# Kernel optimization log

Hardware: AMD Instinct MI355X
Metric: run time of the kernel (lower is better)

## Reference

```python
import jax, jax.numpy as jnp
import numpy as np

EPSILON = 1e-8
DT = 0.1
STEPS = 3
MASK_DENSITY = 0.01


def setup_inputs() -> dict:
    key = jax.random.key(0)
    k1, k2 = jax.random.split(key)
    B, S, D = 4, 4096, 2
    psi = jax.random.normal(k1, (B, S, D), dtype=jnp.float32)
    # binary mask: threshold a uniform draw to get a sparse 0/1 adjacency
    u = jax.random.uniform(k2, (B, S, S), dtype=jnp.float32)
    binary_mask = (u < MASK_DENSITY).astype(jnp.float32)
    return {"psi": psi, "binary_mask": binary_mask}


def reference(psi, binary_mask):
    def force(state):
        # adjacency-weighted aggregation minus self: [B,S,S] @ [B,S,2]
        return jnp.einsum('bij,bjd->bid', binary_mask, state) - state

    def step(p, _):
        r = jnp.linalg.norm(p, axis=-1, keepdims=True)          # [B,S,1]
        k1 = force(p)
        psi_star = p + DT * k1
        star_norm = jnp.linalg.norm(psi_star, axis=-1, keepdims=True)
        psi_star = psi_star * (r / (star_norm + EPSILON))       # renormalize to r
        k2 = force(psi_star)
        p_new = p + 0.5 * DT * (k1 + k2)
        new_norm = jnp.linalg.norm(p_new, axis=-1, keepdims=True)
        p_new = p_new * (r / (new_norm + EPSILON))              # norm-preserving
        return p_new, None

    psi_out, _ = jax.lax.scan(step, psi, None, length=STEPS)
    return psi_out
```

## Files before the change

kernel.cpp:

```cpp
#include <hip/hip_runtime.h>
#include <stdint.h>

#define BATCH   4
#define SEQ     4096
#define WPR     64
#define NROWS   (BATCH * SEQ)
#define CAP     256
#define DTS     0.1f
#define HALF_DT 0.05f
#define EPS     1e-8f

__device__ __forceinline__ float2 ballot_force_sum(unsigned long long w,
                                                   const float2* __restrict__ gb,
                                                   int lane) {
    const int colbase = ((lane >> 2) << 8) | (lane & 3);
    float sx = 0.f, sy = 0.f;
    while (w) {
        int j = __builtin_ctzll(w);
        w &= (w - 1);
        float2 v = gb[colbase + (j << 2)];
        sx += v.x; sy += v.y;
    }
#pragma unroll
    for (int m = 32; m >= 1; m >>= 1) {
        sx += __shfl_xor(sx, m, 64);
        sy += __shfl_xor(sy, m, 64);
    }
    return make_float2(sx, sy);
}

__global__ __launch_bounds__(256)
void compress_phaseA(const float* __restrict__ mask,
                     const float2* __restrict__ psi,
                     ushort* __restrict__ idx,
                     int*    __restrict__ cnt,
                     float2* __restrict__ k1buf,
                     float2* __restrict__ starbuf,
                     float*  __restrict__ rbuf) {
    const int row  = (blockIdx.x * blockDim.x + threadIdx.x) >> 6;
    const int lane = threadIdx.x & 63;

    const float4* src = reinterpret_cast<const float4*>(mask + (size_t)row * SEQ);
    unsigned long long word = 0ull;
#pragma unroll
    for (int c = 0; c < 16; ++c) {
        float4 v = src[c * 64 + lane];
        unsigned long long b;
        b = __ballot(v.x != 0.f); if (lane == c * 4 + 0) word = b;
        b = __ballot(v.y != 0.f); if (lane == c * 4 + 1) word = b;
        b = __ballot(v.z != 0.f); if (lane == c * 4 + 2) word = b;
        b = __ballot(v.w != 0.f); if (lane == c * 4 + 3) word = b;
    }

    int pc  = __popcll(word);
    int inc = pc;
#pragma unroll
    for (int ofs = 1; ofs < 64; ofs <<= 1) {
        int t = __shfl_up(inc, ofs, 64);
        if (lane >= ofs) inc += t;
    }
    int pos   = inc - pc;
    int total = __shfl(inc, 63, 64);

    ushort* dst = idx + ((size_t)row << 8);
    const int colbase = ((lane >> 2) << 8) | (lane & 3);
    unsigned long long w = word;
    while (w) {
        int j = __builtin_ctzll(w);
        w &= (w - 1);
        if (pos < CAP) dst[pos] = (ushort)(colbase + (j << 2));
        ++pos;
    }
    if (lane == 0) cnt[row] = total > CAP ? CAP : total;

    const int bidx = row >> 12;
    float2 sum = ballot_force_sum(word, psi + ((size_t)bidx << 12), lane);
    float2 p  = psi[row];
    float r   = sqrtf(p.x * p.x + p.y * p.y);
    float k1x = sum.x - p.x, k1y = sum.y - p.y;
    float tx  = p.x + DTS * k1x, ty = p.y + DTS * k1y;
    float sc  = r / (sqrtf(tx * tx + ty * ty) + EPS);
    if (lane == 0) {
        k1buf[row]   = make_float2(k1x, k1y);
        starbuf[row] = make_float2(tx * sc, ty * sc);
        rbuf[row]    = r;
    }
}

template <int PHASE>
__global__ __launch_bounds__(256)
void force_step(const ushort* __restrict__ idx,
                const int*    __restrict__ cnt,
                const float2* __restrict__ pIn,
                const float2* __restrict__ gsrc,
                float2* __restrict__ k1buf,
                float2* __restrict__ starbuf,
                float*  __restrict__ rbuf,
                float2* __restrict__ outbuf) {
    const int tid = blockIdx.x * blockDim.x + threadIdx.x;
    const int row = tid >> 4;
    const int q   = tid & 15;
    const int bidx = row >> 12;
    const float2* __restrict__ gb = gsrc + ((size_t)bidx << 12);

    const int n = cnt[row];
    const ushort* __restrict__ ip = idx + ((size_t)row << 8);

    float sx = 0.f, sy = 0.f;
    int i = q;
    for (; i + 16 < n; i += 32) {
        int c0 = ip[i];
        int c1 = ip[i + 16];
        float2 v0 = gb[c0];
        float2 v1 = gb[c1];
        sx += v0.x + v1.x;
        sy += v0.y + v1.y;
    }
    if (i < n) {
        int c = ip[i];
        float2 v = gb[c];
        sx += v.x; sy += v.y;
    }
#pragma unroll
    for (int m = 8; m >= 1; m >>= 1) {
        sx += __shfl_xor(sx, m, 64);
        sy += __shfl_xor(sy, m, 64);
    }

    if (q == 0) {
        if (PHASE == 0) {
            float2 p = pIn[row];
            float r   = sqrtf(p.x * p.x + p.y * p.y);
            float k1x = sx - p.x, k1y = sy - p.y;
            float tx  = p.x + DTS * k1x, ty = p.y + DTS * k1y;
            float sc  = r / (sqrtf(tx * tx + ty * ty) + EPS);
            k1buf[row]   = make_float2(k1x, k1y);
            starbuf[row] = make_float2(tx * sc, ty * sc);
            rbuf[row]    = r;
        } else {
            float2 st = gsrc[row];
            float k2x = sx - st.x, k2y = sy - st.y;
            float2 p  = pIn[row];
            float2 k1 = k1buf[row];
            float nx  = p.x + HALF_DT * (k1.x + k2x);
            float ny  = p.y + HALF_DT * (k1.y + k2y);
            float sc  = rbuf[row] / (sqrtf(nx * nx + ny * ny) + EPS);
            outbuf[row] = make_float2(nx * sc, ny * sc);
        }
    }
}

extern "C" void kernel_launch(void* const* d_in, const int* in_sizes, int n_in,
                              void* d_out, int out_size, void* d_ws, size_t ws_size,
                              hipStream_t stream) {
    const float* psi  = (const float*)d_in[0];
    const float* mask = (const float*)d_in[1];
    float2* out2 = (float2*)d_out;

    char* ws = (char*)d_ws;
    ushort* idx = (ushort*)ws;
    int*    cnt = (int*)(ws + (size_t)NROWS * CAP * sizeof(ushort));
    float2* p    = (float2*)((char*)cnt + (size_t)NROWS * sizeof(int));
    float2* k1   = p + NROWS;
    float2* star = k1 + NROWS;
    float*  rbuf = (float*)(star + NROWS);

    const float2* psi2 = (const float2*)psi;
    const int gridC = NROWS / 4;
    const int gridF = NROWS / 16;

    compress_phaseA<<<gridC, 256, 0, stream>>>(mask, psi2, idx, cnt, k1, star, rbuf);
    force_step<1><<<gridF, 256, 0, stream>>>(idx, cnt, psi2, star, k1, star, rbuf, p);
    force_step<0><<<gridF, 256, 0, stream>>>(idx, cnt, p, p, k1, star, rbuf, nullptr);
    force_step<1><<<gridF, 256, 0, stream>>>(idx, cnt, p, star, k1, star, rbuf, p);
    force_step<0><<<gridF, 256, 0, stream>>>(idx, cnt, p, p, k1, star, rbuf, nullptr);
    force_step<1><<<gridF, 256, 0, stream>>>(idx, cnt, p, star, k1, star, rbuf, out2);
}
```

Measured before the change: 380.5 us.

## Fuse compression and all RK steps into one persistent kernel with grid barriers

Replaces the six kernel launches with a single persistent kernel of 512 blocks. It compresses the mask into sparse column indices, then runs all three integration steps, separated by software grid barriers built on an atomic counter and spin-waiting. k1 and r now stay in registers rather than round-tripping through global buffers. The fused first-step force from the compress kernel is dropped, so that force is recomputed from the compressed index list. The design assumes all 512 blocks are co-resident, and it adds a memset plus spin-barrier overhead.

```diff
diff --git a/kernel.cpp b/kernel.cpp
--- a/kernel.cpp
+++ b/kernel.cpp
@@ -3,109 +3,31 @@
 
 #define BATCH   4
 #define SEQ     4096
-#define WPR     64
 #define NROWS   (BATCH * SEQ)
 #define CAP     256
 #define DTS     0.1f
 #define HALF_DT 0.05f
 #define EPS     1e-8f
 
-__device__ __forceinline__ float2 ballot_force_sum(unsigned long long w,
-                                                   const float2* __restrict__ gb,
-                                                   int lane) {
-    const int colbase = ((lane >> 2) << 8) | (lane & 3);
-    float sx = 0.f, sy = 0.f;
-    while (w) {
-        int j = __builtin_ctzll(w);
-        w &= (w - 1);
-        float2 v = gb[colbase + (j << 2)];
-        sx += v.x; sy += v.y;
+#define NB      512
+#define NT      512
+
+__device__ __forceinline__ void gridbar(int* __restrict__ bar, int gen) {
+    __threadfence();
+    __syncthreads();
+    if (threadIdx.x == 0) {
+        atomicAdd(bar, 1);
+        while (__hip_atomic_load(bar, __ATOMIC_RELAXED,
+                                 __HIP_MEMORY_SCOPE_AGENT) < gen * NB) {
+            __builtin_amdgcn_s_sleep(2);
+        }
     }
-#pragma unroll
-    for (int m = 32; m >= 1; m >>= 1) {
-        sx += __shfl_xor(sx, m, 64);
-        sy += __shfl_xor(sy, m, 64);
-    }
-    return make_float2(sx, sy);
+    __syncthreads();
+    __threadfence();
 }
 
-__global__ __launch_bounds__(256)
-void compress_phaseA(const float* __restrict__ mask,
-                     const float2* __restrict__ psi,
-                     ushort* __restrict__ idx,
-                     int*    __restrict__ cnt,
-                     float2* __restrict__ k1buf,
-                     float2* __restrict__ starbuf,
-                     float*  __restrict__ rbuf) {
-    const int row  = (blockIdx.x * blockDim.x + threadIdx.x) >> 6;
-    const int lane = threadIdx.x & 63;
-
-    const float4* src = reinterpret_cast<const float4*>(mask + (size_t)row * SEQ);
-    unsigned long long word = 0ull;
-#pragma unroll
-    for (int c = 0; c < 16; ++c) {
-        float4 v = src[c * 64 + lane];
-        unsigned long long b;
-        b = __ballot(v.x != 0.f); if (lane == c * 4 + 0) word = b;
-        b = __ballot(v.y != 0.f); if (lane == c * 4 + 1) word = b;
-        b = __ballot(v.z != 0.f); if (lane == c * 4 + 2) word = b;
-        b = __ballot(v.w != 0.f); if (lane == c * 4 + 3) word = b;
-    }
-
-    int pc  = __popcll(word);
-    int inc = pc;
-#pragma unroll
-    for (int ofs = 1; ofs < 64; ofs <<= 1) {
-        int t = __shfl_up(inc, ofs, 64);
-        if (lane >= ofs) inc += t;
-    }
-    int pos   = inc - pc;
-    int total = __shfl(inc, 63, 64);
-
-    ushort* dst = idx + ((size_t)row << 8);
-    const int colbase = ((lane >> 2) << 8) | (lane & 3);
-    unsigned long long w = word;
-    while (w) {
-        int j = __builtin_ctzll(w);
-        w &= (w - 1);
-        if (pos < CAP) dst[pos] = (ushort)(colbase + (j << 2));
-        ++pos;
-    }
-    if (lane == 0) cnt[row] = total > CAP ? CAP : total;
-
-    const int bidx = row >> 12;
-    float2 sum = ballot_force_sum(word, psi + ((size_t)bidx << 12), lane);
-    float2 p  = psi[row];
-    float r   = sqrtf(p.x * p.x + p.y * p.y);
-    float k1x = sum.x - p.x, k1y = sum.y - p.y;
-    float tx  = p.x + DTS * k1x, ty = p.y + DTS * k1y;
-    float sc  = r / (sqrtf(tx * tx + ty * ty) + EPS);
-    if (lane == 0) {
-        k1buf[row]   = make_float2(k1x, k1y);
-        starbuf[row] = make_float2(tx * sc, ty * sc);
-        rbuf[row]    = r;
-    }
-}
-
-template <int PHASE>
-__global__ __launch_bounds__(256)
-void force_step(const ushort* __restrict__ idx,
-                const int*    __restrict__ cnt,
-                const float2* __restrict__ pIn,
-                const float2* __restrict__ gsrc,
-                float2* __restrict__ k1buf,
-                float2* __restrict__ starbuf,
-                float*  __restrict__ rbuf,
-                float2* __restrict__ outbuf) {
-    const int tid = blockIdx.x * blockDim.x + threadIdx.x;
-    const int row = tid >> 4;
-    const int q   = tid & 15;
-    const int bidx = row >> 12;
-    const float2* __restrict__ gb = gsrc + ((size_t)bidx << 12);
-
-    const int n = cnt[row];
-    const ushort* __restrict__ ip = idx + ((size_t)row << 8);
-
+__device__ __forceinline__ float2 gather16(const ushort* __restrict__ ip, int n,
+                                           const float2* __restrict__ gb, int q) {
     float sx = 0.f, sy = 0.f;
     int i = q;
     for (; i + 16 < n; i += 32) {
@@ -126,26 +48,99 @@
         sx += __shfl_xor(sx, m, 64);
         sy += __shfl_xor(sy, m, 64);
     }
+    return make_float2(sx, sy);
+}
 
-    if (q == 0) {
-        if (PHASE == 0) {
-            float2 p = pIn[row];
-            float r   = sqrtf(p.x * p.x + p.y * p.y);
-            float k1x = sx - p.x, k1y = sy - p.y;
-            float tx  = p.x + DTS * k1x, ty = p.y + DTS * k1y;
-            float sc  = r / (sqrtf(tx * tx + ty * ty) + EPS);
-            k1buf[row]   = make_float2(k1x, k1y);
-            starbuf[row] = make_float2(tx * sc, ty * sc);
-            rbuf[row]    = r;
+__global__ __launch_bounds__(NT)
+void fused(const float* __restrict__ mask,
+           const float2* __restrict__ psi,
+           ushort* __restrict__ idx,
+           int*    __restrict__ cnt,
+           float2* __restrict__ pbuf,
+           float2* __restrict__ star,
+           float2* __restrict__ out,
+           int*    __restrict__ bar) {
+    const int tid  = blockIdx.x * NT + threadIdx.x;
+    const int lane = threadIdx.x & 63;
+
+    {
+        const int gw = tid >> 6;
+#pragma unroll 1
+        for (int rr = 0; rr < 4; ++rr) {
+            const int row = gw * 4 + rr;
+            const float4* src = reinterpret_cast<const float4*>(mask + (size_t)row * SEQ);
+            unsigned long long word = 0ull;
+#pragma unroll
+            for (int c = 0; c < 16; ++c) {
+                float4 v = src[c * 64 + lane];
+                unsigned long long b;
+                b = __ballot(v.x != 0.f); if (lane == c * 4 + 0) word = b;
+                b = __ballot(v.y != 0.f); if (lane == c * 4 + 1) word = b;
+                b = __ballot(v.z != 0.f); if (lane == c * 4 + 2) word = b;
+                b = __ballot(v.w != 0.f); if (lane == c * 4 + 3) word = b;
+            }
+            int pc  = __popcll(word);
+            int inc = pc;
+#pragma unroll
+            for (int ofs = 1; ofs < 64; ofs <<= 1) {
+                int t = __shfl_up(inc, ofs, 64);
+                if (lane >= ofs) inc += t;
+            }
+            int pos   = inc - pc;
+            int total = __shfl(inc, 63, 64);
+            ushort* dst = idx + ((size_t)row << 8);
+            const int colbase = ((lane >> 2) << 8) | (lane & 3);
+            unsigned long long w = word;
+            while (w) {
+                int j = __builtin_ctzll(w);
+                w &= (w - 1);
+                if (pos < CAP) dst[pos] = (ushort)(colbase + (j << 2));
+                ++pos;
+            }
+            if (lane == 0) cnt[row] = total > CAP ? CAP : total;
+        }
+    }
+
+    gridbar(bar, 1);
+
+    const int row = tid >> 4;
+    const int q   = tid & 15;
+    const int bidx = row >> 12;
+    const float2* __restrict__ psiB  = psi  + ((size_t)bidx << 12);
+    const float2* __restrict__ pbufB = pbuf + ((size_t)bidx << 12);
+    const float2* __restrict__ starB = star + ((size_t)bidx << 12);
+
+    const int n = cnt[row];
+    const ushort* __restrict__ ip = idx + ((size_t)row << 8);
+
+    float2 p = psi[row];
+    int gen = 1;
+
+#pragma unroll 1
+    for (int step = 0; step < 3; ++step) {
+        const float2* __restrict__ gsA = (step == 0) ? psiB : pbufB;
+        float r = sqrtf(p.x * p.x + p.y * p.y);
+
+        float2 sumA = gather16(ip, n, gsA, q);
+        float k1x = sumA.x - p.x, k1y = sumA.y - p.y;
+        float tx  = p.x + DTS * k1x, ty = p.y + DTS * k1y;
+        float scA = r / (sqrtf(tx * tx + ty * ty) + EPS);
+        float stx = tx * scA, sty = ty * scA;
+        if (q == 0) star[row] = make_float2(stx, sty);
+        gridbar(bar, ++gen);
+
+        float2 sumB = gather16(ip, n, starB, q);
+        float k2x = sumB.x - stx, k2y = sumB.y - sty;
+        float nx  = p.x + HALF_DT * (k1x + k2x);
+        float ny  = p.y + HALF_DT * (k1y + k2y);
+        float scB = r / (sqrtf(nx * nx + ny * ny) + EPS);
+        p = make_float2(nx * scB, ny * scB);
+
+        if (step < 2) {
+            if (q == 0) pbuf[row] = p;
+            gridbar(bar, ++gen);
         } else {
-            float2 st = gsrc[row];
-            float k2x = sx - st.x, k2y = sy - st.y;
-            float2 p  = pIn[row];
-            float2 k1 = k1buf[row];
-            float nx  = p.x + HALF_DT * (k1.x + k2x);
-            float ny  = p.y + HALF_DT * (k1.y + k2y);
-            float sc  = rbuf[row] / (sqrtf(nx * nx + ny * ny) + EPS);
-            outbuf[row] = make_float2(nx * sc, ny * sc);
+            if (q == 0) out[row] = p;
         }
     }
 }
@@ -158,21 +153,13 @@
     float2* out2 = (float2*)d_out;
 
     char* ws = (char*)d_ws;
-    ushort* idx = (ushort*)ws;
-    int*    cnt = (int*)(ws + (size_t)NROWS * CAP * sizeof(ushort));
-    float2* p    = (float2*)((char*)cnt + (size_t)NROWS * sizeof(int));
-    float2* k1   = p + NROWS;
-    float2* star = k1 + NROWS;
-    float*  rbuf = (float*)(star + NROWS);
+    int*    bar = (int*)ws;
+    ushort* idx = (ushort*)(ws + 256);
+    int*    cnt = (int*)((char*)idx + (size_t)NROWS * CAP * sizeof(ushort));
+    float2* pbuf = (float2*)((char*)cnt + (size_t)NROWS * sizeof(int));
+    float2* star = pbuf + NROWS;
 
-    const float2* psi2 = (const float2*)psi;
-    const int gridC = NROWS / 4;
-    const int gridF = NROWS / 16;
-
-    compress_phaseA<<<gridC, 256, 0, stream>>>(mask, psi2, idx, cnt, k1, star, rbuf);
-    force_step<1><<<gridF, 256, 0, stream>>>(idx, cnt, psi2, star, k1, star, rbuf, p);
-    force_step<0><<<gridF, 256, 0, stream>>>(idx, cnt, p, p, k1, star, rbuf, nullptr);
-    force_step<1><<<gridF, 256, 0, stream>>>(idx, cnt, p, star, k1, star, rbuf, p);
-    force_step<0><<<gridF, 256, 0, stream>>>(idx, cnt, p, p, k1, star, rbuf, nullptr);
-    force_step<1><<<gridF, 256, 0, stream>>>(idx, cnt, p, star, k1, star, rbuf, out2);
+    hipMemsetAsync(bar, 0, 64, stream);
+    fused<<<NB, NT, 0, stream>>>(mask, (const float2*)psi, idx, cnt,
+                                 pbuf, star, out2, bar);
 }
```

Result: slower. 1.294 ms (+240.2%).

## Batch mask loads in compress and use one wavefront per row in force steps

Applied to the files above, without the earlier changes.

The compress kernel now issues all 16 float4 loads of a mask row before the ballot loop, so more memory requests are in flight per wave. The force-step kernels change from 16 threads per row to a full 64-lane wavefront per row, with a 6-level shuffle reduction. Per-row operands are loaded before the gather loop so their latency overlaps with it. The aim is shorter per-row loops and better latency hiding, at the cost of 4x more waves for the same work and longer reductions, with many lanes idle at about 41 neighbours per row.

```diff
diff --git a/kernel.cpp b/kernel.cpp
--- a/kernel.cpp
+++ b/kernel.cpp
@@ -3,7 +3,6 @@
 
 #define BATCH   4
 #define SEQ     4096
-#define WPR     64
 #define NROWS   (BATCH * SEQ)
 #define CAP     256
 #define DTS     0.1f
@@ -41,15 +40,18 @@
     const int lane = threadIdx.x & 63;
 
     const float4* src = reinterpret_cast<const float4*>(mask + (size_t)row * SEQ);
+    float4 v[16];
+#pragma unroll
+    for (int c = 0; c < 16; ++c) v[c] = src[c * 64 + lane];
+
     unsigned long long word = 0ull;
 #pragma unroll
     for (int c = 0; c < 16; ++c) {
-        float4 v = src[c * 64 + lane];
         unsigned long long b;
-        b = __ballot(v.x != 0.f); if (lane == c * 4 + 0) word = b;
-        b = __ballot(v.y != 0.f); if (lane == c * 4 + 1) word = b;
-        b = __ballot(v.z != 0.f); if (lane == c * 4 + 2) word = b;
-        b = __ballot(v.w != 0.f); if (lane == c * 4 + 3) word = b;
+        b = __ballot(v[c].x != 0.f); if (lane == c * 4 + 0) word = b;
+        b = __ballot(v[c].y != 0.f); if (lane == c * 4 + 1) word = b;
+        b = __ballot(v[c].z != 0.f); if (lane == c * 4 + 2) word = b;
+        b = __ballot(v[c].w != 0.f); if (lane == c * 4 + 3) word = b;
     }
 
     int pc  = __popcll(word);
@@ -97,56 +99,46 @@
                 float2* __restrict__ starbuf,
                 float*  __restrict__ rbuf,
                 float2* __restrict__ outbuf) {
-    const int tid = blockIdx.x * blockDim.x + threadIdx.x;
-    const int row = tid >> 4;
-    const int q   = tid & 15;
+    const int row  = (blockIdx.x * blockDim.x + threadIdx.x) >> 6;
+    const int lane = threadIdx.x & 63;
     const int bidx = row >> 12;
     const float2* __restrict__ gb = gsrc + ((size_t)bidx << 12);
 
     const int n = cnt[row];
     const ushort* __restrict__ ip = idx + ((size_t)row << 8);
 
+    float2 p = pIn[row];
+    float2 st = make_float2(0.f, 0.f), k1 = make_float2(0.f, 0.f);
+    float  rv = 0.f;
+    if (PHASE == 1) { st = gsrc[row]; k1 = k1buf[row]; rv = rbuf[row]; }
+
     float sx = 0.f, sy = 0.f;
-    int i = q;
-    for (; i + 16 < n; i += 32) {
-        int c0 = ip[i];
-        int c1 = ip[i + 16];
-        float2 v0 = gb[c0];
-        float2 v1 = gb[c1];
-        sx += v0.x + v1.x;
-        sy += v0.y + v1.y;
-    }
-    if (i < n) {
-        int c = ip[i];
-        float2 v = gb[c];
+    for (int i = lane; i < n; i += 64) {
+        float2 v = gb[ip[i]];
         sx += v.x; sy += v.y;
     }
 #pragma unroll
-    for (int m = 8; m >= 1; m >>= 1) {
+    for (int m = 32; m >= 1; m >>= 1) {
         sx += __shfl_xor(sx, m, 64);
         sy += __shfl_xor(sy, m, 64);
     }
 
-    if (q == 0) {
-        if (PHASE == 0) {
-            float2 p = pIn[row];
-            float r   = sqrtf(p.x * p.x + p.y * p.y);
-            float k1x = sx - p.x, k1y = sy - p.y;
-            float tx  = p.x + DTS * k1x, ty = p.y + DTS * k1y;
-            float sc  = r / (sqrtf(tx * tx + ty * ty) + EPS);
+    if (PHASE == 0) {
+        float r   = sqrtf(p.x * p.x + p.y * p.y);
+        float k1x = sx - p.x, k1y = sy - p.y;
+        float tx  = p.x + DTS * k1x, ty = p.y + DTS * k1y;
+        float sc  = r / (sqrtf(tx * tx + ty * ty) + EPS);
+        if (lane == 0) {
             k1buf[row]   = make_float2(k1x, k1y);
             starbuf[row] = make_float2(tx * sc, ty * sc);
             rbuf[row]    = r;
-        } else {
-            float2 st = gsrc[row];
-            float k2x = sx - st.x, k2y = sy - st.y;
-            float2 p  = pIn[row];
-            float2 k1 = k1buf[row];
-            float nx  = p.x + HALF_DT * (k1.x + k2x);
-            float ny  = p.y + HALF_DT * (k1.y + k2y);
-            float sc  = rbuf[row] / (sqrtf(nx * nx + ny * ny) + EPS);
-            outbuf[row] = make_float2(nx * sc, ny * sc);
         }
+    } else {
+        float k2x = sx - st.x, k2y = sy - st.y;
+        float nx  = p.x + HALF_DT * (k1.x + k2x);
+        float ny  = p.y + HALF_DT * (k1.y + k2y);
+        float sc  = rv / (sqrtf(nx * nx + ny * ny) + EPS);
+        if (lane == 0) outbuf[row] = make_float2(nx * sc, ny * sc);
     }
 }
 
@@ -166,13 +158,12 @@
     float*  rbuf = (float*)(star + NROWS);
 
     const float2* psi2 = (const float2*)psi;
-    const int gridC = NROWS / 4;
-    const int gridF = NROWS / 16;
+    const int grid = NROWS / 4;
 
-    compress_phaseA<<<gridC, 256, 0, stream>>>(mask, psi2, idx, cnt, k1, star, rbuf);
-    force_step<1><<<gridF, 256, 0, stream>>>(idx, cnt, psi2, star, k1, star, rbuf, p);
-    force_step<0><<<gridF, 256, 0, stream>>>(idx, cnt, p, p, k1, star, rbuf, nullptr);
-    force_step<1><<<gridF, 256, 0, stream>>>(idx, cnt, p, star, k1, star, rbuf, p);
-    force_step<0><<<gridF, 256, 0, stream>>>(idx, cnt, p, p, k1, star, rbuf, nullptr);
-    force_step<1><<<gridF, 256, 0, stream>>>(idx, cnt, p, star, k1, star, rbuf, out2);
+    compress_phaseA<<<grid, 256, 0, stream>>>(mask, psi2, idx, cnt, k1, star, rbuf);
+    force_step<1><<<grid, 256, 0, stream>>>(idx, cnt, psi2, star, k1, star, rbuf, p);
+    force_step<0><<<grid, 256, 0, stream>>>(idx, cnt, p, p, k1, star, rbuf, nullptr);
+    force_step<1><<<grid, 256, 0, stream>>>(idx, cnt, p, star, k1, star, rbuf, p);
+    force_step<0><<<grid, 256, 0, stream>>>(idx, cnt, p, p, k1, star, rbuf, nullptr);
+    force_step<1><<<grid, 256, 0, stream>>>(idx, cnt, p, star, k1, star, rbuf, out2);
 }
```

Measured after the change: 389.7 us. 2.4% more time.

## Fuse five force-step launches into one LDS-resident per-batch integrate kernel

Applied to the files above, without the earlier changes.

Replaces the five separate force_step launches with a single integrate kernel: one 1024-thread block per batch, holding the psi, star, k1 and r vectors for that batch in shared memory. It runs all remaining RK2 phases of the three steps with block-wide barriers, so the state never goes back to global memory between phases. The neighbour index list per row shrinks from 256 to 80 slots, which cuts index storage and traffic but silently truncates rows that have more than 80 nonzeros. The mask is also read with nontemporal loads. The cost is that only four workgroups occupy the GPU, so the gather loops rely on latency hiding within a single CU per batch.

```diff
diff --git a/kernel.cpp b/kernel.cpp
--- a/kernel.cpp
+++ b/kernel.cpp
@@ -3,12 +3,13 @@
 
 #define BATCH   4
 #define SEQ     4096
-#define WPR     64
 #define NROWS   (BATCH * SEQ)
-#define CAP     256
+#define SLOTS   80
 #define DTS     0.1f
 #define HALF_DT 0.05f
 #define EPS     1e-8f
+
+typedef float fx4 __attribute__((ext_vector_type(4)));
 
 __device__ __forceinline__ float2 ballot_force_sum(unsigned long long w,
                                                    const float2* __restrict__ gb,
@@ -40,11 +41,11 @@
     const int row  = (blockIdx.x * blockDim.x + threadIdx.x) >> 6;
     const int lane = threadIdx.x & 63;
 
-    const float4* src = reinterpret_cast<const float4*>(mask + (size_t)row * SEQ);
+    const fx4* src = reinterpret_cast<const fx4*>(mask + (size_t)row * SEQ);
     unsigned long long word = 0ull;
 #pragma unroll
     for (int c = 0; c < 16; ++c) {
-        float4 v = src[c * 64 + lane];
+        fx4 v = __builtin_nontemporal_load(&src[c * 64 + lane]);
         unsigned long long b;
         b = __ballot(v.x != 0.f); if (lane == c * 4 + 0) word = b;
         b = __ballot(v.y != 0.f); if (lane == c * 4 + 1) word = b;
@@ -62,16 +63,16 @@
     int pos   = inc - pc;
     int total = __shfl(inc, 63, 64);
 
-    ushort* dst = idx + ((size_t)row << 8);
+    ushort* dst = idx + (size_t)row * SLOTS;
     const int colbase = ((lane >> 2) << 8) | (lane & 3);
     unsigned long long w = word;
     while (w) {
         int j = __builtin_ctzll(w);
         w &= (w - 1);
-        if (pos < CAP) dst[pos] = (ushort)(colbase + (j << 2));
+        if (pos < SLOTS) dst[pos] = (ushort)(colbase + (j << 2));
         ++pos;
     }
-    if (lane == 0) cnt[row] = total > CAP ? CAP : total;
+    if (lane == 0) cnt[row] = total > SLOTS ? SLOTS : total;
 
     const int bidx = row >> 12;
     float2 sum = ballot_force_sum(word, psi + ((size_t)bidx << 12), lane);
@@ -82,71 +83,101 @@
     float sc  = r / (sqrtf(tx * tx + ty * ty) + EPS);
     if (lane == 0) {
         k1buf[row]   = make_float2(k1x, k1y);
+        rbuf[row]    = r;
         starbuf[row] = make_float2(tx * sc, ty * sc);
-        rbuf[row]    = r;
-    }
-}
-
-template <int PHASE>
-__global__ __launch_bounds__(256)
-void force_step(const ushort* __restrict__ idx,
-                const int*    __restrict__ cnt,
-                const float2* __restrict__ pIn,
-                const float2* __restrict__ gsrc,
-                float2* __restrict__ k1buf,
-                float2* __restrict__ starbuf,
-                float*  __restrict__ rbuf,
-                float2* __restrict__ outbuf) {
-    const int tid = blockIdx.x * blockDim.x + threadIdx.x;
-    const int row = tid >> 4;
-    const int q   = tid & 15;
-    const int bidx = row >> 12;
-    const float2* __restrict__ gb = gsrc + ((size_t)bidx << 12);
-
-    const int n = cnt[row];
-    const ushort* __restrict__ ip = idx + ((size_t)row << 8);
-
-    float sx = 0.f, sy = 0.f;
-    int i = q;
-    for (; i + 16 < n; i += 32) {
-        int c0 = ip[i];
-        int c1 = ip[i + 16];
-        float2 v0 = gb[c0];
-        float2 v1 = gb[c1];
-        sx += v0.x + v1.x;
-        sy += v0.y + v1.y;
-    }
-    if (i < n) {
-        int c = ip[i];
-        float2 v = gb[c];
-        sx += v.x; sy += v.y;
-    }
-#pragma unroll
-    for (int m = 8; m >= 1; m >>= 1) {
-        sx += __shfl_xor(sx, m, 64);
-        sy += __shfl_xor(sy, m, 64);
-    }
-
-    if (q == 0) {
-        if (PHASE == 0) {
-            float2 p = pIn[row];
-            float r   = sqrtf(p.x * p.x + p.y * p.y);
-            float k1x = sx - p.x, k1y = sy - p.y;
-            float tx  = p.x + DTS * k1x, ty = p.y + DTS * k1y;
-            float sc  = r / (sqrtf(tx * tx + ty * ty) + EPS);
-            k1buf[row]   = make_float2(k1x, k1y);
-            starbuf[row] = make_float2(tx * sc, ty * sc);
-            rbuf[row]    = r;
-        } else {
-            float2 st = gsrc[row];
-            float k2x = sx - st.x, k2y = sy - st.y;
-            float2 p  = pIn[row];
-            float2 k1 = k1buf[row];
-            float nx  = p.x + HALF_DT * (k1.x + k2x);
-            float ny  = p.y + HALF_DT * (k1.y + k2y);
-            float sc  = rbuf[row] / (sqrtf(nx * nx + ny * ny) + EPS);
-            outbuf[row] = make_float2(nx * sc, ny * sc);
+    }
+}
+
+__global__ __launch_bounds__(1024)
+void integrate(const ushort* __restrict__ idx,
+               const int*    __restrict__ cnt,
+               const float2* __restrict__ psi,
+               const float2* __restrict__ starG,
+               const float2* __restrict__ k1G,
+               const float*  __restrict__ rG,
+               float2* __restrict__ out) {
+    __shared__ float2 P[SEQ];
+    __shared__ float2 ST[SEQ];
+    __shared__ float2 K1[SEQ];
+    __shared__ float  RR[SEQ];
+
+    const int    t  = threadIdx.x;
+    const int    q  = t & 15;
+    const int    g  = t >> 4;
+    const size_t bo = (size_t)blockIdx.x << 12;
+
+    {
+        const float4* s;
+        float4* d;
+        s = reinterpret_cast<const float4*>(psi + bo);  d = reinterpret_cast<float4*>(P);
+        d[t] = s[t]; d[t + 1024] = s[t + 1024];
+        s = reinterpret_cast<const float4*>(starG + bo); d = reinterpret_cast<float4*>(ST);
+        d[t] = s[t]; d[t + 1024] = s[t + 1024];
+        s = reinterpret_cast<const float4*>(k1G + bo);  d = reinterpret_cast<float4*>(K1);
+        d[t] = s[t]; d[t + 1024] = s[t + 1024];
+        s = reinterpret_cast<const float4*>(rG + bo);   d = reinterpret_cast<float4*>(RR);
+        d[t] = s[t];
+    }
+    __syncthreads();
+
+#pragma unroll 1
+    for (int step = 0; step < 3; ++step) {
+        for (int pass = 0; pass < 64; ++pass) {
+            const int row = pass * 64 + g;
+            const int n = cnt[bo + row];
+            const ushort* __restrict__ ip = idx + (bo + row) * SLOTS;
+            float sx = 0.f, sy = 0.f;
+            for (int i = q; i < n; i += 16) {
+                float2 v = ST[ip[i]];
+                sx += v.x; sy += v.y;
+            }
+#pragma unroll
+            for (int m = 8; m >= 1; m >>= 1) {
+                sx += __shfl_xor(sx, m, 64);
+                sy += __shfl_xor(sy, m, 64);
+            }
+            if (q == 0) {
+                float2 st = ST[row];
+                float2 p  = P[row];
+                float2 k1 = K1[row];
+                float k2x = sx - st.x, k2y = sy - st.y;
+                float nx  = p.x + HALF_DT * (k1.x + k2x);
+                float ny  = p.y + HALF_DT * (k1.y + k2y);
+                float sc  = RR[row] / (sqrtf(nx * nx + ny * ny) + EPS);
+                float2 pn = make_float2(nx * sc, ny * sc);
+                if (step == 2) out[bo + row] = pn;
+                else          P[row] = pn;
+            }
         }
+        if (step == 2) break;
+        __syncthreads();
+
+        for (int pass = 0; pass < 64; ++pass) {
+            const int row = pass * 64 + g;
+            const int n = cnt[bo + row];
+            const ushort* __restrict__ ip = idx + (bo + row) * SLOTS;
+            float sx = 0.f, sy = 0.f;
+            for (int i = q; i < n; i += 16) {
+                float2 v = P[ip[i]];
+                sx += v.x; sy += v.y;
+            }
+#pragma unroll
+            for (int m = 8; m >= 1; m >>= 1) {
+                sx += __shfl_xor(sx, m, 64);
+                sy += __shfl_xor(sy, m, 64);
+            }
+            if (q == 0) {
+                float2 p  = P[row];
+                float r   = sqrtf(p.x * p.x + p.y * p.y);
+                float k1x = sx - p.x, k1y = sy - p.y;
+                float tx  = p.x + DTS * k1x, ty = p.y + DTS * k1y;
+                float sc  = r / (sqrtf(tx * tx + ty * ty) + EPS);
+                K1[row] = make_float2(k1x, k1y);
+                RR[row] = r;
+                ST[row] = make_float2(tx * sc, ty * sc);
+            }
+        }
+        __syncthreads();
     }
 }
 
@@ -158,21 +189,15 @@
     float2* out2 = (float2*)d_out;
 
     char* ws = (char*)d_ws;
-    ushort* idx = (ushort*)ws;
-    int*    cnt = (int*)(ws + (size_t)NROWS * CAP * sizeof(ushort));
-    float2* p    = (float2*)((char*)cnt + (size_t)NROWS * sizeof(int));
-    float2* k1   = p + NROWS;
-    float2* star = k1 + NROWS;
-    float*  rbuf = (float*)(star + NROWS);
+    ushort* idx  = (ushort*)ws;
+    int*    cnt  = (int*)(ws + (size_t)NROWS * SLOTS * sizeof(ushort));
+    float2* star = (float2*)((char*)cnt + (size_t)NROWS * sizeof(int));
+    float2* k1   = star + NROWS;
+    float*  rbuf = (float*)(k1 + NROWS);
 
     const float2* psi2 = (const float2*)psi;
-    const int gridC = NROWS / 4;
-    const int gridF = NROWS / 16;
-
-    compress_phaseA<<<gridC, 256, 0, stream>>>(mask, psi2, idx, cnt, k1, star, rbuf);
-    force_step<1><<<gridF, 256, 0, stream>>>(idx, cnt, psi2, star, k1, star, rbuf, p);
-    force_step<0><<<gridF, 256, 0, stream>>>(idx, cnt, p, p, k1, star, rbuf, nullptr);
-    force_step<1><<<gridF, 256, 0, stream>>>(idx, cnt, p, star, k1, star, rbuf, p);
-    force_step<0><<<gridF, 256, 0, stream>>>(idx, cnt, p, p, k1, star, rbuf, nullptr);
-    force_step<1><<<gridF, 256, 0, stream>>>(idx, cnt, p, star, k1, star, rbuf, out2);
-}
+
+    compress_phaseA<<<NROWS / 4, 256, 0, stream>>>(mask, psi2, idx, cnt,
+                                                   k1, star, rbuf);
+    integrate<<<BATCH, 1024, 0, stream>>>(idx, cnt, psi2, star, k1, rbuf, out2);
+}
```

New measurement: 705.6 us. +85.5%, slower.
